# Optimization experiments

Hardware: AMD Instinct MI355X
Metric: run time of the kernel (lower is better)

## Reference

```python
import jax, jax.numpy as jnp
import numpy as np

B, S, D, H = 2, 2048, 1024, 16
HD = D // H  # per-head dim = 64


def setup_inputs() -> dict:
    key = jax.random.key(0)
    ks = jax.random.split(key, 9)
    s = 0.02
    return {
        "h": jax.random.normal(ks[0], (B, S, D), jnp.float32),
        "Wq": jax.random.normal(ks[1], (D, D), jnp.float32) * s,
        "bq": jax.random.normal(ks[2], (D,), jnp.float32) * s,
        "Wk": jax.random.normal(ks[3], (D, D), jnp.float32) * s,
        "bk": jax.random.normal(ks[4], (D,), jnp.float32) * s,
        "Wv": jax.random.normal(ks[5], (D, D), jnp.float32) * s,
        "bv": jax.random.normal(ks[6], (D,), jnp.float32) * s,
        "Wo": jax.random.normal(ks[7], (D, D), jnp.float32) * s,
        "bo": jax.random.normal(ks[8], (D,), jnp.float32) * s,
    }


def reference(h, Wq, bq, Wk, bk, Wv, bv, Wo, bo):
    b, s, d = h.shape
    # Linear projections (torch Linear: x @ W.T + b), split heads -> [B,H,S,HD]
    def split_heads(x):
        return x.reshape(b, s, H, HD).transpose(0, 2, 1, 3)

    q = split_heads(h @ Wq.T + bq)
    k = split_heads(h @ Wk.T + bk)
    v = split_heads(h @ Wv.T + bv)

    # scaled scores [B,H,S,S]
    qk = jnp.einsum("bhqd,bhkd->bhqk", q, k) / np.sqrt(HD).astype(np.float32)
    # causal mask: strictly upper triangle -> -inf
    causal = jnp.triu(jnp.ones((s, s), dtype=bool), k=1)
    qk = jnp.where(causal[None, None], -jnp.inf, qk)

    probs = jax.nn.softmax(qk, axis=-1)
    o = jnp.einsum("bhqk,bhkd->bhqd", probs, v)
    o = o.transpose(0, 2, 1, 3).reshape(b, s, d)
    return o @ Wo.T + bo
```

## Files before the change

### kernel.cpp

```cpp
#include <hip/hip_runtime.h>
#include <stdint.h>

typedef __bf16 bf16;
typedef __bf16 bf16x4_t __attribute__((ext_vector_type(4)));
typedef __bf16 bf16x8_t __attribute__((ext_vector_type(8)));
typedef float f32x4 __attribute__((ext_vector_type(4)));

static constexpr int NB = 2, SS = 2048, DD = 1024, NH = 16, HD = 64;

__device__ __forceinline__ void gl_lds16(const void* g, void* l) {
    __builtin_amdgcn_global_load_lds((__attribute__((address_space(1))) void*)g,
                                     (__attribute__((address_space(3))) void*)l, 16, 0, 0);
}

__global__ __launch_bounds__(256) void cast_all(const float* __restrict__ h,
                                                const float* __restrict__ Wq,
                                                const float* __restrict__ Wk,
                                                const float* __restrict__ Wv,
                                                const float* __restrict__ Wo,
                                                bf16* __restrict__ dst) {
    int i = blockIdx.x * 256 + threadIdx.x;
    const float* src;
    int off;
    if (i < 1048576) { src = h; off = i; }
    else {
        int r = i - 1048576;
        int w = r >> 18;
        off = r & 262143;
        src = (w == 0) ? Wq : (w == 1) ? Wk : (w == 2) ? Wv : Wo;
    }
    float4 v = reinterpret_cast<const float4*>(src)[off];
    bf16x4_t o;
    o.x = (bf16)v.x; o.y = (bf16)v.y; o.z = (bf16)v.z; o.w = (bf16)v.w;
    reinterpret_cast<bf16x4_t*>(dst)[i] = o;
}

__device__ __forceinline__ void gemm128_mainloop(const bf16* __restrict__ Ablk,
                                                 const bf16* __restrict__ Bblk,
                                                 int K, f32x4 acc[4][4]) {
    __shared__ __align__(16) bf16 As[128 * 32];
    __shared__ __align__(16) bf16 Bs[128 * 32];
    const int tid = threadIdx.x;
    const int wave = tid >> 6, lane = tid & 63;
    const int quad = lane >> 4, l15 = lane & 15;
    const int wm = wave >> 1, wn = wave & 1;

#pragma unroll
    for (int mi = 0; mi < 4; mi++)
#pragma unroll
        for (int ni = 0; ni < 4; ni++) {
            acc[mi][ni][0] = 0.f; acc[mi][ni][1] = 0.f;
            acc[mi][ni][2] = 0.f; acc[mi][ni][3] = 0.f;
        }

    const int n0c = tid;
    const int r0 = n0c >> 2, c0 = (n0c & 3) ^ ((r0 >> 1) & 3);
    const int n1c = 256 + tid;
    const int r1 = n1c >> 2, c1 = (n1c & 3) ^ ((r1 >> 1) & 3);

    for (int kk = 0; kk < K; kk += 32) {
        __syncthreads();
        gl_lds16(Ablk + (size_t)r0 * K + kk + c0 * 8, &As[(wave * 64) * 8]);
        gl_lds16(Ablk + (size_t)r1 * K + kk + c1 * 8, &As[(256 + wave * 64) * 8]);
        gl_lds16(Bblk + (size_t)r0 * K + kk + c0 * 8, &Bs[(wave * 64) * 8]);
        gl_lds16(Bblk + (size_t)r1 * K + kk + c1 * 8, &Bs[(256 + wave * 64) * 8]);
        __syncthreads();

        bf16x8_t a[4], b[4];
#pragma unroll
        for (int mi = 0; mi < 4; mi++) {
            int R = wm * 64 + mi * 16 + l15;
            a[mi] = *(const bf16x8_t*)&As[R * 32 + ((quad ^ ((R >> 1) & 3)) << 3)];
        }
#pragma unroll
        for (int ni = 0; ni < 4; ni++) {
            int R = wn * 64 + ni * 16 + l15;
            b[ni] = *(const bf16x8_t*)&Bs[R * 32 + ((quad ^ ((R >> 1) & 3)) << 3)];
        }
#pragma unroll
        for (int mi = 0; mi < 4; mi++)
#pragma unroll
            for (int ni = 0; ni < 4; ni++)
                acc[mi][ni] = __builtin_amdgcn_mfma_f32_16x16x32_bf16(a[mi], b[ni], acc[mi][ni], 0, 0, 0);
    }
}

__device__ __forceinline__ void gemm64_mainloop(const bf16* __restrict__ Ablk,
                                                const bf16* __restrict__ Bblk,
                                                int K, f32x4 acc[2][4]) {
    __shared__ __align__(16) bf16 As[64 * 32];
    __shared__ __align__(16) bf16 Bs[128 * 32];
    const int tid = threadIdx.x;
    const int wave = tid >> 6, lane = tid & 63;
    const int quad = lane >> 4, l15 = lane & 15;
    const int wm = wave >> 1, wn = wave & 1;

#pragma unroll
    for (int mi = 0; mi < 2; mi++)
#pragma unroll
        for (int ni = 0; ni < 4; ni++) {
            acc[mi][ni][0] = 0.f; acc[mi][ni][1] = 0.f;
            acc[mi][ni][2] = 0.f; acc[mi][ni][3] = 0.f;
        }

    const int ra = tid >> 2, ca = (tid & 3) ^ ((ra >> 1) & 3);
    const int r0 = tid >> 2, c0 = (tid & 3) ^ ((r0 >> 1) & 3);
    const int n1c = 256 + tid;
    const int r1 = n1c >> 2, c1 = (n1c & 3) ^ ((r1 >> 1) & 3);

    for (int kk = 0; kk < K; kk += 32) {
        __syncthreads();
        gl_lds16(Ablk + (size_t)ra * K + kk + ca * 8, &As[(wave * 64) * 8]);
        gl_lds16(Bblk + (size_t)r0 * K + kk + c0 * 8, &Bs[(wave * 64) * 8]);
        gl_lds16(Bblk + (size_t)r1 * K + kk + c1 * 8, &Bs[(256 + wave * 64) * 8]);
        __syncthreads();

        bf16x8_t a[2], b[4];
#pragma unroll
        for (int mi = 0; mi < 2; mi++) {
            int R = wm * 32 + mi * 16 + l15;
            a[mi] = *(const bf16x8_t*)&As[R * 32 + ((quad ^ ((R >> 1) & 3)) << 3)];
        }
#pragma unroll
        for (int ni = 0; ni < 4; ni++) {
            int R = wn * 64 + ni * 16 + l15;
            b[ni] = *(const bf16x8_t*)&Bs[R * 32 + ((quad ^ ((R >> 1) & 3)) << 3)];
        }
#pragma unroll
        for (int mi = 0; mi < 2; mi++)
#pragma unroll
            for (int ni = 0; ni < 4; ni++)
                acc[mi][ni] = __builtin_amdgcn_mfma_f32_16x16x32_bf16(a[mi], b[ni], acc[mi][ni], 0, 0, 0);
    }
}

__global__ __launch_bounds__(256) void gemm_qkv(const bf16* __restrict__ A, const bf16* __restrict__ Wqkv,
                                                const float* __restrict__ bq, const float* __restrict__ bk,
                                                const float* __restrict__ bv,
                                                bf16* __restrict__ Qb, bf16* __restrict__ Kb, bf16* __restrict__ Vb) {
    const int m0 = blockIdx.x * 128;
    const int n0 = blockIdx.y * 128;
    f32x4 acc[4][4];
    gemm128_mainloop(A + (size_t)m0 * DD, Wqkv + (size_t)n0 * DD, DD, acc);

    const int tid = threadIdx.x, wave = tid >> 6, lane = tid & 63;
    const int quad = lane >> 4, l15 = lane & 15;
    const int wm = wave >> 1, wn = wave & 1;

    const int which = n0 >> 10;
    const float* bias = (which == 0) ? bq : (which == 1) ? bk : bv;
    const float sc = (which == 0) ? 0.18033688f : 1.0f;

    const int cbase = (n0 & 1023) + wn * 64;
    const int head = cbase >> 6;
    const int bb = m0 >> 11;
    const int s0 = (m0 & 2047) + wm * 64;

    if (which == 2) {
        bf16* dbase = Vb + ((size_t)(bb * NH + head)) * HD * SS;
#pragma unroll
        for (int ni = 0; ni < 4; ni++) {
            float bsv = bias[cbase + ni * 16 + l15];
            int hd = ni * 16 + l15;
#pragma unroll
            for (int mi = 0; mi < 4; mi++) {
                bf16x4_t pb;
                pb.x = (bf16)(acc[mi][ni][0] + bsv);
                pb.y = (bf16)(acc[mi][ni][1] + bsv);
                pb.z = (bf16)(acc[mi][ni][2] + bsv);
                pb.w = (bf16)(acc[mi][ni][3] + bsv);
                int s = s0 + mi * 16 + quad * 4;
                *(bf16x4_t*)&dbase[(size_t)hd * SS + s] = pb;
            }
        }
    } else {
        bf16* dst = (which == 0) ? Qb : Kb;
        bf16* dbase = dst + ((size_t)(bb * NH + head)) * SS * HD;
#pragma unroll
        for (int ni = 0; ni < 4; ni++) {
            float bsv = bias[cbase + ni * 16 + l15];
            int hd = ni * 16 + l15;
#pragma unroll
            for (int mi = 0; mi < 4; mi++) {
#pragma unroll
                for (int r = 0; r < 4; r++) {
                    int s = s0 + mi * 16 + quad * 4 + r;
                    dbase[(size_t)s * HD + hd] = (bf16)((acc[mi][ni][r] + bsv) * sc);
                }
            }
        }
    }
}

__global__ __launch_bounds__(256) void gemm_out(const bf16* __restrict__ A, const bf16* __restrict__ Wo,
                                                const float* __restrict__ bo, float* __restrict__ out) {
    const int m0 = blockIdx.x * 64, n0 = blockIdx.y * 128;
    f32x4 acc[2][4];
    gemm64_mainloop(A + (size_t)m0 * DD, Wo + (size_t)n0 * DD, DD, acc);

    const int tid = threadIdx.x, wave = tid >> 6, lane = tid & 63;
    const int quad = lane >> 4, l15 = lane & 15;
    const int wm = wave >> 1, wn = wave & 1;
    float* obase = out + (size_t)(m0 + wm * 32) * DD + n0 + wn * 64;
#pragma unroll
    for (int ni = 0; ni < 4; ni++) {
        float bias = bo[n0 + wn * 64 + ni * 16 + l15];
#pragma unroll
        for (int mi = 0; mi < 2; mi++)
#pragma unroll
            for (int r = 0; r < 4; r++)
                obase[(size_t)(mi * 16 + quad * 4 + r) * DD + ni * 16 + l15] = acc[mi][ni][r] + bias;
    }
}

__global__ __launch_bounds__(256, 3) void attn_kernel(const bf16* __restrict__ Qb, const bf16* __restrict__ Kb,
                                                      const bf16* __restrict__ Vb, bf16* __restrict__ Ob,
                                                      bf16* __restrict__ Opart, float* __restrict__ Ml) {
    constexpr int PQ[24]  = {15,14,13,12,11,10, 9, 8, 15, 7, 14, 6, 13, 5, 12, 4, 11, 3, 10, 2,  9, 1,  8, 0};
    constexpr int PJ0[24] = { 0, 0, 0, 0, 0, 0, 0, 0,  8, 0,  8, 0,  8, 0,  8, 0,  8, 0,  8, 0,  8, 0,  8, 0};
    constexpr int PJ1[24] = { 8, 8, 8, 8, 8, 8, 8, 8, 16, 8, 15, 7, 14, 6, 13, 5, 12, 4, 11, 3, 10, 2,  9, 1};

    __shared__ __align__(16) bf16 Kt[128 * 64];
    __shared__ __align__(16) bf16 Vt[64 * 128];
    __shared__ __align__(16) bf16 Pt[4 * 32 * 64];

    const int tid = threadIdx.x, wave = tid >> 6, lane = tid & 63;
    const int quad = lane >> 4, l15 = lane & 15;
    const int bx = blockIdx.x;
    const int p = bx >> 5, bh = bx & 31;
    const int qtile = PQ[p], jbeg = PJ0[p], jend = PJ1[p];
    const bool diagpart = (jend == qtile + 1);
    const size_t hoff = (size_t)bh * SS * HD;
    const bf16* Qg = Qb + hoff + (size_t)qtile * 128 * HD;
    const bf16* Vbase = Vb + (size_t)bh * HD * SS;
    bf16* Pw = &Pt[wave * 2048];

    bf16x8_t qf[2][2];
#pragma unroll
    for (int qt = 0; qt < 2; qt++)
#pragma unroll
        for (int ks = 0; ks < 2; ks++)
            qf[qt][ks] = *(const bf16x8_t*)(Qg + (wave * 32 + qt * 16 + l15) * HD + ks * 32 + quad * 8);

    f32x4 o[2][4];
#pragma unroll
    for (int qt = 0; qt < 2; qt++)
#pragma unroll
        for (int nO = 0; nO < 4; nO++) {
            o[qt][nO][0] = 0.f; o[qt][nO][1] = 0.f; o[qt][nO][2] = 0.f; o[qt][nO][3] = 0.f;
        }
    float mrow[2] = {-__builtin_inff(), -__builtin_inff()};
    float lrow[2] = {0.f, 0.f};

    for (int j = jbeg; j < jend; j++) {
        __syncthreads();
        const bf16* Kg = Kb + hoff + (size_t)j * 128 * HD;
#pragma unroll
        for (int t = 0; t < 4; t++) {
            int n = t * 256 + tid;
            int row = n >> 3, gc = (n & 7) ^ (row & 7);
            gl_lds16(Kg + row * HD + gc * 8, &Kt[(t * 256 + wave * 64) * 8]);
        }
        const bf16* Vg = Vbase + j * 128;
#pragma unroll
        for (int t = 0; t < 4; t++) {
            int n = t * 256 + tid;
            int row = n >> 4, gc = (n & 15) ^ (row & 15);
            gl_lds16(Vg + (size_t)row * SS + gc * 8, &Vt[(t * 256 + wave * 64) * 8]);
        }
        __syncthreads();

        const bool diag = diagpart && (j == jend - 1);
#pragma unroll 1
        for (int kh = 0; kh < 2; kh++) {
            if (diag && kh == 1 && wave < 2) break;

            f32x4 st[4][2];
#pragma unroll
            for (int kt = 0; kt < 4; kt++)
#pragma unroll
                for (int qt = 0; qt < 2; qt++) {
                    st[kt][qt][0] = 0.f; st[kt][qt][1] = 0.f; st[kt][qt][2] = 0.f; st[kt][qt][3] = 0.f;
                }
#pragma unroll
            for (int ks = 0; ks < 2; ks++) {
#pragma unroll
                for (int kt = 0; kt < 4; kt++) {
                    int R = (kh * 4 + kt) * 16 + l15;
                    bf16x8_t kf = *(const bf16x8_t*)&Kt[R * HD + ((((ks << 2) | quad) ^ (R & 7)) << 3)];
#pragma unroll
                    for (int qt = 0; qt < 2; qt++)
                        st[kt][qt] = __builtin_amdgcn_mfma_f32_16x16x32_bf16(kf, qf[qt][ks], st[kt][qt], 0, 0, 0);
                }
            }
            if (diag) {
#pragma unroll
                for (int kt = 0; kt < 4; kt++)
#pragma unroll
                    for (int qt = 0; qt < 2; qt++)
#pragma unroll
                        for (int r = 0; r < 4; r++) {
                            int key = kh * 64 + kt * 16 + quad * 4 + r;
                            int row = wave * 32 + qt * 16 + l15;
                            if (key > row) st[kt][qt][r] = -__builtin_inff();
                        }
            }

#pragma unroll
            for (int qt = 0; qt < 2; qt++) {
                float mx = -__builtin_inff();
#pragma unroll
                for (int kt = 0; kt < 4; kt++)
#pragma unroll
                    for (int r = 0; r < 4; r++) mx = fmaxf(mx, st[kt][qt][r]);
                mx = fmaxf(mx, __shfl_xor(mx, 16));
                mx = fmaxf(mx, __shfl_xor(mx, 32));
                float mnew = fmaxf(mrow[qt], mx);
                float alpha = exp2f(mrow[qt] - mnew);
                mrow[qt] = mnew;
                float sum = 0.f;
                const int row = qt * 16 + l15;
#pragma unroll
                for (int kt = 0; kt < 4; kt++) {
                    float p0 = exp2f(st[kt][qt][0] - mnew);
                    float p1 = exp2f(st[kt][qt][1] - mnew);
                    float p2 = exp2f(st[kt][qt][2] - mnew);
                    float p3 = exp2f(st[kt][qt][3] - mnew);
                    sum += (p0 + p1) + (p2 + p3);
                    bf16x4_t pb;
                    pb.x = (bf16)p0; pb.y = (bf16)p1; pb.z = (bf16)p2; pb.w = (bf16)p3;
                    int c = kt * 2 + (quad >> 1);
                    *(bf16x4_t*)&Pw[row * 64 + ((c ^ (row & 7)) << 3) + ((quad & 1) << 2)] = pb;
                }
                sum += __shfl_xor(sum, 16);
                sum += __shfl_xor(sum, 32);
                lrow[qt] = lrow[qt] * alpha + sum;
#pragma unroll
                for (int r = 0; r < 4; r++) {
                    float a = __shfl(alpha, (lane & 48) | (quad * 4 + r));
#pragma unroll
                    for (int nO = 0; nO < 4; nO++) o[qt][nO][r] *= a;
                }
            }

#pragma unroll
            for (int ks = 0; ks < 2; ks++) {
                bf16x8_t pf[2];
#pragma unroll
                for (int qt = 0; qt < 2; qt++) {
                    int row = qt * 16 + l15;
                    int c = (ks << 2) | quad;
                    pf[qt] = *(const bf16x8_t*)&Pw[row * 64 + ((c ^ (row & 7)) << 3)];
                }
#pragma unroll
                for (int nO = 0; nO < 4; nO++) {
                    int c = kh * 8 + ks * 4 + quad;
                    bf16x8_t vf = *(const bf16x8_t*)&Vt[(nO * 16 + l15) * 128 + ((c ^ l15) << 3)];
#pragma unroll
                    for (int qt = 0; qt < 2; qt++)
                        o[qt][nO] = __builtin_amdgcn_mfma_f32_16x16x32_bf16(pf[qt], vf, o[qt][nO], 0, 0, 0);
                }
            }
        }
    }

    const int bb = bh >> 4, hh = bh & 15;
    if (qtile >= 8) {
        const int pidx = ((bh << 3) + (qtile - 8)) * 2 + (jbeg != 0 ? 1 : 0);
        bf16* Op = Opart + (size_t)pidx * (128 * 64);
        float* mlp = Ml + (size_t)pidx * 256;
#pragma unroll
        for (int qt = 0; qt < 2; qt++) {
            if (quad == 0) {
                mlp[wave * 32 + qt * 16 + l15] = mrow[qt];
                mlp[128 + wave * 32 + qt * 16 + l15] = lrow[qt];
            }
#pragma unroll
            for (int r = 0; r < 4; r++) {
                int row = wave * 32 + qt * 16 + quad * 4 + r;
#pragma unroll
                for (int nO = 0; nO < 4; nO++)
                    Op[row * 64 + nO * 16 + l15] = (bf16)o[qt][nO][r];
            }
        }
    } else {
#pragma unroll
        for (int qt = 0; qt < 2; qt++) {
#pragma unroll
            for (int r = 0; r < 4; r++) {
                float linv = 1.f / __shfl(lrow[qt], (lane & 48) | (quad * 4 + r));
                int srow = qtile * 128 + wave * 32 + qt * 16 + quad * 4 + r;
#pragma unroll
                for (int nO = 0; nO < 4; nO++)
                    Ob[((size_t)(bb * SS + srow)) * DD + hh * HD + nO * 16 + l15] = (bf16)(o[qt][nO][r] * linv);
            }
        }
    }
}

__global__ __launch_bounds__(256) void merge_kernel(const bf16* __restrict__ Opart,
                                                    const float* __restrict__ Ml,
                                                    bf16* __restrict__ Ob) {
    const int bh = blockIdx.x >> 3, q8 = blockIdx.x & 7;
    const int p0 = ((bh << 3) + q8) * 2, p1 = p0 + 1;
    const int t = threadIdx.x, row = t >> 1, c0 = (t & 1) * 32;
    float m0 = Ml[p0 * 256 + row], l0 = Ml[p0 * 256 + 128 + row];
    float m1 = Ml[p1 * 256 + row], l1 = Ml[p1 * 256 + 128 + row];
    float M = fmaxf(m0, m1);
    float w0 = exp2f(m0 - M), w1 = exp2f(m1 - M);
    float inv = 1.f / (l0 * w0 + l1 * w1);
    w0 *= inv; w1 *= inv;
    const bf16* O0 = Opart + (size_t)p0 * (128 * 64) + row * 64 + c0;
    const bf16* O1 = Opart + (size_t)p1 * (128 * 64) + row * 64 + c0;
    const int bb = bh >> 4, hh = bh & 15;
    const int srow = (8 + q8) * 128 + row;
    bf16* dst = Ob + ((size_t)(bb * SS + srow)) * DD + hh * HD + c0;
#pragma unroll
    for (int i = 0; i < 4; i++) {
        bf16x8_t a = *(const bf16x8_t*)(O0 + i * 8);
        bf16x8_t b = *(const bf16x8_t*)(O1 + i * 8);
        bf16x8_t r;
#pragma unroll
        for (int jj = 0; jj < 8; jj++)
            r[jj] = (bf16)((float)a[jj] * w0 + (float)b[jj] * w1);
        *(bf16x8_t*)(dst + i * 8) = r;
    }
}

extern "C" void kernel_launch(void* const* d_in, const int* in_sizes, int n_in,
                              void* d_out, int out_size, void* d_ws, size_t ws_size,
                              hipStream_t stream) {
    (void)in_sizes; (void)n_in; (void)out_size; (void)ws_size;
    const float* h  = (const float*)d_in[0];
    const float* Wq = (const float*)d_in[1];
    const float* bq = (const float*)d_in[2];
    const float* Wk = (const float*)d_in[3];
    const float* bk = (const float*)d_in[4];
    const float* Wv = (const float*)d_in[5];
    const float* bv = (const float*)d_in[6];
    const float* Wo = (const float*)d_in[7];
    const float* bo = (const float*)d_in[8];
    float* out = (float*)d_out;

    char* ws = (char*)d_ws;
    bf16* hbf  = (bf16*)(ws);
    bf16* wqkv = (bf16*)(ws + 8388608);
    bf16* wo   = (bf16*)(ws + 8388608 + 6291456);
    bf16* Qb   = (bf16*)(ws + 16777216);
    bf16* Kb   = (bf16*)(ws + 16777216 + 8388608);
    bf16* Vb   = (bf16*)(ws + 16777216 + 2 * 8388608);
    bf16* Ob   = (bf16*)(ws + 16777216 + 3 * 8388608);
    bf16*  Opart = (bf16*)(ws);
    float* Ml    = (float*)(ws + 8388608);

    cast_all<<<8192, 256, 0, stream>>>(h, Wq, Wk, Wv, Wo, hbf);
    gemm_qkv<<<dim3(32, 24), 256, 0, stream>>>(hbf, wqkv, bq, bk, bv, Qb, Kb, Vb);
    attn_kernel<<<768, 256, 0, stream>>>(Qb, Kb, Vb, Ob, Opart, Ml);
    merge_kernel<<<256, 256, 0, stream>>>(Opart, Ml, Ob);
    gemm_out<<<dim3(64, 8), 256, 0, stream>>>(Ob, wo, bo, out);
}
```

Measured before the change: 187.9 us.

## Deepen GEMM K-tile to 64 and transpose PV MFMA for vectorized epilogue

```diff
diff --git a/kernel.cpp b/kernel.cpp
--- a/kernel.cpp
+++ b/kernel.cpp
@@ -38,8 +38,8 @@
 __device__ __forceinline__ void gemm128_mainloop(const bf16* __restrict__ Ablk,
                                                  const bf16* __restrict__ Bblk,
                                                  int K, f32x4 acc[4][4]) {
-    __shared__ __align__(16) bf16 As[128 * 32];
-    __shared__ __align__(16) bf16 Bs[128 * 32];
+    __shared__ __align__(16) bf16 As[128 * 64];
+    __shared__ __align__(16) bf16 Bs[128 * 64];
     const int tid = threadIdx.x;
     const int wave = tid >> 6, lane = tid & 63;
     const int quad = lane >> 4, l15 = lane & 15;
@@ -53,43 +53,50 @@
             acc[mi][ni][2] = 0.f; acc[mi][ni][3] = 0.f;
         }
 
-    const int n0c = tid;
-    const int r0 = n0c >> 2, c0 = (n0c & 3) ^ ((r0 >> 1) & 3);
-    const int n1c = 256 + tid;
-    const int r1 = n1c >> 2, c1 = (n1c & 3) ^ ((r1 >> 1) & 3);
-
-    for (int kk = 0; kk < K; kk += 32) {
+    int rr[4], cc[4];
+#pragma unroll
+    for (int n = 0; n < 4; n++) {
+        int cid = n * 256 + tid;
+        rr[n] = cid >> 3;
+        cc[n] = (cid & 7) ^ (rr[n] & 7);
+    }
+
+    for (int kk = 0; kk < K; kk += 64) {
         __syncthreads();
-        gl_lds16(Ablk + (size_t)r0 * K + kk + c0 * 8, &As[(wave * 64) * 8]);
-        gl_lds16(Ablk + (size_t)r1 * K + kk + c1 * 8, &As[(256 + wave * 64) * 8]);
-        gl_lds16(Bblk + (size_t)r0 * K + kk + c0 * 8, &Bs[(wave * 64) * 8]);
-        gl_lds16(Bblk + (size_t)r1 * K + kk + c1 * 8, &Bs[(256 + wave * 64) * 8]);
+#pragma unroll
+        for (int n = 0; n < 4; n++) {
+            gl_lds16(Ablk + (size_t)rr[n] * K + kk + cc[n] * 8, &As[(n * 256 + wave * 64) * 8]);
+            gl_lds16(Bblk + (size_t)rr[n] * K + kk + cc[n] * 8, &Bs[(n * 256 + wave * 64) * 8]);
+        }
         __syncthreads();
 
-        bf16x8_t a[4], b[4];
-#pragma unroll
-        for (int mi = 0; mi < 4; mi++) {
-            int R = wm * 64 + mi * 16 + l15;
-            a[mi] = *(const bf16x8_t*)&As[R * 32 + ((quad ^ ((R >> 1) & 3)) << 3)];
-        }
-#pragma unroll
-        for (int ni = 0; ni < 4; ni++) {
-            int R = wn * 64 + ni * 16 + l15;
-            b[ni] = *(const bf16x8_t*)&Bs[R * 32 + ((quad ^ ((R >> 1) & 3)) << 3)];
-        }
-#pragma unroll
-        for (int mi = 0; mi < 4; mi++)
-#pragma unroll
-            for (int ni = 0; ni < 4; ni++)
-                acc[mi][ni] = __builtin_amdgcn_mfma_f32_16x16x32_bf16(a[mi], b[ni], acc[mi][ni], 0, 0, 0);
+#pragma unroll
+        for (int ks = 0; ks < 2; ks++) {
+            bf16x8_t a[4], b[4];
+#pragma unroll
+            for (int mi = 0; mi < 4; mi++) {
+                int R = wm * 64 + mi * 16 + l15;
+                a[mi] = *(const bf16x8_t*)&As[R * 64 + ((((ks << 2) | quad) ^ (R & 7)) << 3)];
+            }
+#pragma unroll
+            for (int ni = 0; ni < 4; ni++) {
+                int R = wn * 64 + ni * 16 + l15;
+                b[ni] = *(const bf16x8_t*)&Bs[R * 64 + ((((ks << 2) | quad) ^ (R & 7)) << 3)];
+            }
+#pragma unroll
+            for (int mi = 0; mi < 4; mi++)
+#pragma unroll
+                for (int ni = 0; ni < 4; ni++)
+                    acc[mi][ni] = __builtin_amdgcn_mfma_f32_16x16x32_bf16(a[mi], b[ni], acc[mi][ni], 0, 0, 0);
+        }
     }
 }
 
 __device__ __forceinline__ void gemm64_mainloop(const bf16* __restrict__ Ablk,
                                                 const bf16* __restrict__ Bblk,
                                                 int K, f32x4 acc[2][4]) {
-    __shared__ __align__(16) bf16 As[64 * 32];
-    __shared__ __align__(16) bf16 Bs[128 * 32];
+    __shared__ __align__(16) bf16 As[64 * 64];
+    __shared__ __align__(16) bf16 Bs[128 * 64];
     const int tid = threadIdx.x;
     const int wave = tid >> 6, lane = tid & 63;
     const int quad = lane >> 4, l15 = lane & 15;
@@ -103,34 +110,49 @@
             acc[mi][ni][2] = 0.f; acc[mi][ni][3] = 0.f;
         }
 
-    const int ra = tid >> 2, ca = (tid & 3) ^ ((ra >> 1) & 3);
-    const int r0 = tid >> 2, c0 = (tid & 3) ^ ((r0 >> 1) & 3);
-    const int n1c = 256 + tid;
-    const int r1 = n1c >> 2, c1 = (n1c & 3) ^ ((r1 >> 1) & 3);
-
-    for (int kk = 0; kk < K; kk += 32) {
+    int ra[2], ca[2], rb[4], cb[4];
+#pragma unroll
+    for (int n = 0; n < 2; n++) {
+        int cid = n * 256 + tid;
+        ra[n] = cid >> 3;
+        ca[n] = (cid & 7) ^ (ra[n] & 7);
+    }
+#pragma unroll
+    for (int n = 0; n < 4; n++) {
+        int cid = n * 256 + tid;
+        rb[n] = cid >> 3;
+        cb[n] = (cid & 7) ^ (rb[n] & 7);
+    }
+
+    for (int kk = 0; kk < K; kk += 64) {
         __syncthreads();
-        gl_lds16(Ablk + (size_t)ra * K + kk + ca * 8, &As[(wave * 64) * 8]);
-        gl_lds16(Bblk + (size_t)r0 * K + kk + c0 * 8, &Bs[(wave * 64) * 8]);
-        gl_lds16(Bblk + (size_t)r1 * K + kk + c1 * 8, &Bs[(256 + wave * 64) * 8]);
+#pragma unroll
+        for (int n = 0; n < 2; n++)
+            gl_lds16(Ablk + (size_t)ra[n] * K + kk + ca[n] * 8, &As[(n * 256 + wave * 64) * 8]);
+#pragma unroll
+        for (int n = 0; n < 4; n++)
+            gl_lds16(Bblk + (size_t)rb[n] * K + kk + cb[n] * 8, &Bs[(n * 256 + wave * 64) * 8]);
         __syncthreads();
 
-        bf16x8_t a[2], b[4];
-#pragma unroll
-        for (int mi = 0; mi < 2; mi++) {
-            int R = wm * 32 + mi * 16 + l15;
-            a[mi] = *(const bf16x8_t*)&As[R * 32 + ((quad ^ ((R >> 1) & 3)) << 3)];
-        }
-#pragma unroll
-        for (int ni = 0; ni < 4; ni++) {
-            int R = wn * 64 + ni * 16 + l15;
-            b[ni] = *(const bf16x8_t*)&Bs[R * 32 + ((quad ^ ((R >> 1) & 3)) << 3)];
-        }
-#pragma unroll
-        for (int mi = 0; mi < 2; mi++)
-#pragma unroll
-            for (int ni = 0; ni < 4; ni++)
-                acc[mi][ni] = __builtin_amdgcn_mfma_f32_16x16x32_bf16(a[mi], b[ni], acc[mi][ni], 0, 0, 0);
+#pragma unroll
+        for (int ks = 0; ks < 2; ks++) {
+            bf16x8_t a[2], b[4];
+#pragma unroll
+            for (int mi = 0; mi < 2; mi++) {
+                int R = wm * 32 + mi * 16 + l15;
+                a[mi] = *(const bf16x8_t*)&As[R * 64 + ((((ks << 2) | quad) ^ (R & 7)) << 3)];
+            }
+#pragma unroll
+            for (int ni = 0; ni < 4; ni++) {
+                int R = wn * 64 + ni * 16 + l15;
+                b[ni] = *(const bf16x8_t*)&Bs[R * 64 + ((((ks << 2) | quad) ^ (R & 7)) << 3)];
+            }
+#pragma unroll
+            for (int mi = 0; mi < 2; mi++)
+#pragma unroll
+                for (int ni = 0; ni < 4; ni++)
+                    acc[mi][ni] = __builtin_amdgcn_mfma_f32_16x16x32_bf16(a[mi], b[ni], acc[mi][ni], 0, 0, 0);
+        }
     }
 }
 
@@ -246,8 +268,8 @@
 #pragma unroll
     for (int qt = 0; qt < 2; qt++)
 #pragma unroll
-        for (int nO = 0; nO < 4; nO++) {
-            o[qt][nO][0] = 0.f; o[qt][nO][1] = 0.f; o[qt][nO][2] = 0.f; o[qt][nO][3] = 0.f;
+        for (int dt = 0; dt < 4; dt++) {
+            o[qt][dt][0] = 0.f; o[qt][dt][1] = 0.f; o[qt][dt][2] = 0.f; o[qt][dt][3] = 0.f;
         }
     float mrow[2] = {-__builtin_inff(), -__builtin_inff()};
     float lrow[2] = {0.f, 0.f};
@@ -336,11 +358,7 @@
                 sum += __shfl_xor(sum, 32);
                 lrow[qt] = lrow[qt] * alpha + sum;
 #pragma unroll
-                for (int r = 0; r < 4; r++) {
-                    float a = __shfl(alpha, (lane & 48) | (quad * 4 + r));
-#pragma unroll
-                    for (int nO = 0; nO < 4; nO++) o[qt][nO][r] *= a;
-                }
+                for (int dt = 0; dt < 4; dt++) o[qt][dt] *= alpha;
             }
 
 #pragma unroll
@@ -353,46 +371,69 @@
                     pf[qt] = *(const bf16x8_t*)&Pw[row * 64 + ((c ^ (row & 7)) << 3)];
                 }
 #pragma unroll
-                for (int nO = 0; nO < 4; nO++) {
+                for (int dt = 0; dt < 4; dt++) {
                     int c = kh * 8 + ks * 4 + quad;
-                    bf16x8_t vf = *(const bf16x8_t*)&Vt[(nO * 16 + l15) * 128 + ((c ^ l15) << 3)];
+                    bf16x8_t vf = *(const bf16x8_t*)&Vt[(dt * 16 + l15) * 128 + ((c ^ l15) << 3)];
 #pragma unroll
                     for (int qt = 0; qt < 2; qt++)
-                        o[qt][nO] = __builtin_amdgcn_mfma_f32_16x16x32_bf16(pf[qt], vf, o[qt][nO], 0, 0, 0);
+                        o[qt][dt] = __builtin_amdgcn_mfma_f32_16x16x32_bf16(vf, pf[qt], o[qt][dt], 0, 0, 0);
                 }
             }
         }
     }
 
     const int bb = bh >> 4, hh = bh & 15;
-    if (qtile >= 8) {
+    const bool split = (qtile >= 8);
+    float scl[2];
+#pragma unroll
+    for (int qt = 0; qt < 2; qt++) scl[qt] = split ? 1.f : (1.f / lrow[qt]);
+
+    if (split) {
         const int pidx = ((bh << 3) + (qtile - 8)) * 2 + (jbeg != 0 ? 1 : 0);
-        bf16* Op = Opart + (size_t)pidx * (128 * 64);
         float* mlp = Ml + (size_t)pidx * 256;
-#pragma unroll
-        for (int qt = 0; qt < 2; qt++) {
-            if (quad == 0) {
+        if (quad == 0) {
+#pragma unroll
+            for (int qt = 0; qt < 2; qt++) {
                 mlp[wave * 32 + qt * 16 + l15] = mrow[qt];
                 mlp[128 + wave * 32 + qt * 16 + l15] = lrow[qt];
             }
-#pragma unroll
-            for (int r = 0; r < 4; r++) {
-                int row = wave * 32 + qt * 16 + quad * 4 + r;
-#pragma unroll
-                for (int nO = 0; nO < 4; nO++)
-                    Op[row * 64 + nO * 16 + l15] = (bf16)o[qt][nO][r];
-            }
-        }
-    } else {
-#pragma unroll
-        for (int qt = 0; qt < 2; qt++) {
-#pragma unroll
-            for (int r = 0; r < 4; r++) {
-                float linv = 1.f / __shfl(lrow[qt], (lane & 48) | (quad * 4 + r));
-                int srow = qtile * 128 + wave * 32 + qt * 16 + quad * 4 + r;
-#pragma unroll
-                for (int nO = 0; nO < 4; nO++)
-                    Ob[((size_t)(bb * SS + srow)) * DD + hh * HD + nO * 16 + l15] = (bf16)(o[qt][nO][r] * linv);
+        }
+    }
+#pragma unroll
+    for (int qt = 0; qt < 2; qt++) {
+        const int row = qt * 16 + l15;
+#pragma unroll
+        for (int dt = 0; dt < 4; dt++) {
+            bf16x4_t pb;
+            pb.x = (bf16)(o[qt][dt][0] * scl[qt]);
+            pb.y = (bf16)(o[qt][dt][1] * scl[qt]);
+            pb.z = (bf16)(o[qt][dt][2] * scl[qt]);
+            pb.w = (bf16)(o[qt][dt][3] * scl[qt]);
+            int c = dt * 2 + (quad >> 1);
+            *(bf16x4_t*)&Pw[row * 64 + ((c ^ (row & 7)) << 3) + ((quad & 1) << 2)] = pb;
+        }
+    }
+    {
+        const int rl = lane >> 1;
+        const int half = lane & 1;
+        const int q = wave * 32 + rl;
+        if (split) {
+            const int pidx = ((bh << 3) + (qtile - 8)) * 2 + (jbeg != 0 ? 1 : 0);
+            bf16* Op = Opart + (size_t)pidx * (128 * 64);
+#pragma unroll
+            for (int i = 0; i < 4; i++) {
+                int dc = half * 4 + i;
+                bf16x8_t v = *(const bf16x8_t*)&Pw[rl * 64 + ((dc ^ (rl & 7)) << 3)];
+                *(bf16x8_t*)&Op[q * 64 + dc * 8] = v;
+            }
+        } else {
+            const int srow = qtile * 128 + q;
+            bf16* dst = Ob + ((size_t)(bb * SS + srow)) * DD + hh * HD;
+#pragma unroll
+            for (int i = 0; i < 4; i++) {
+                int dc = half * 4 + i;
+                bf16x8_t v = *(const bf16x8_t*)&Pw[rl * 64 + ((dc ^ (rl & 7)) << 3)];
+                *(bf16x8_t*)&dst[dc * 8] = v;
             }
         }
     }
```

New measurement: 198.2 us. 5.5% more time.

## Fuse split-KV merge into output projection GEMM and swizzle QKV block order

Applied to the files above, without the earlier changes.

```diff
diff --git a/kernel.cpp b/kernel.cpp
--- a/kernel.cpp
+++ b/kernel.cpp
@@ -85,61 +85,16 @@
     }
 }
 
-__device__ __forceinline__ void gemm64_mainloop(const bf16* __restrict__ Ablk,
-                                                const bf16* __restrict__ Bblk,
-                                                int K, f32x4 acc[2][4]) {
-    __shared__ __align__(16) bf16 As[64 * 32];
-    __shared__ __align__(16) bf16 Bs[128 * 32];
-    const int tid = threadIdx.x;
-    const int wave = tid >> 6, lane = tid & 63;
-    const int quad = lane >> 4, l15 = lane & 15;
-    const int wm = wave >> 1, wn = wave & 1;
-
-#pragma unroll
-    for (int mi = 0; mi < 2; mi++)
-#pragma unroll
-        for (int ni = 0; ni < 4; ni++) {
-            acc[mi][ni][0] = 0.f; acc[mi][ni][1] = 0.f;
-            acc[mi][ni][2] = 0.f; acc[mi][ni][3] = 0.f;
-        }
-
-    const int ra = tid >> 2, ca = (tid & 3) ^ ((ra >> 1) & 3);
-    const int r0 = tid >> 2, c0 = (tid & 3) ^ ((r0 >> 1) & 3);
-    const int n1c = 256 + tid;
-    const int r1 = n1c >> 2, c1 = (n1c & 3) ^ ((r1 >> 1) & 3);
-
-    for (int kk = 0; kk < K; kk += 32) {
-        __syncthreads();
-        gl_lds16(Ablk + (size_t)ra * K + kk + ca * 8, &As[(wave * 64) * 8]);
-        gl_lds16(Bblk + (size_t)r0 * K + kk + c0 * 8, &Bs[(wave * 64) * 8]);
-        gl_lds16(Bblk + (size_t)r1 * K + kk + c1 * 8, &Bs[(256 + wave * 64) * 8]);
-        __syncthreads();
-
-        bf16x8_t a[2], b[4];
-#pragma unroll
-        for (int mi = 0; mi < 2; mi++) {
-            int R = wm * 32 + mi * 16 + l15;
-            a[mi] = *(const bf16x8_t*)&As[R * 32 + ((quad ^ ((R >> 1) & 3)) << 3)];
-        }
-#pragma unroll
-        for (int ni = 0; ni < 4; ni++) {
-            int R = wn * 64 + ni * 16 + l15;
-            b[ni] = *(const bf16x8_t*)&Bs[R * 32 + ((quad ^ ((R >> 1) & 3)) << 3)];
-        }
-#pragma unroll
-        for (int mi = 0; mi < 2; mi++)
-#pragma unroll
-            for (int ni = 0; ni < 4; ni++)
-                acc[mi][ni] = __builtin_amdgcn_mfma_f32_16x16x32_bf16(a[mi], b[ni], acc[mi][ni], 0, 0, 0);
-    }
-}
-
 __global__ __launch_bounds__(256) void gemm_qkv(const bf16* __restrict__ A, const bf16* __restrict__ Wqkv,
                                                 const float* __restrict__ bq, const float* __restrict__ bk,
                                                 const float* __restrict__ bv,
                                                 bf16* __restrict__ Qb, bf16* __restrict__ Kb, bf16* __restrict__ Vb) {
-    const int m0 = blockIdx.x * 128;
-    const int n0 = blockIdx.y * 128;
+    const int g = blockIdx.x + 32 * blockIdx.y;
+    const int c = g & 7, i = g >> 3;
+    const int xm = (c & 3) * 8 + (i & 7);
+    const int yn = (c >> 2) * 12 + (i >> 3);
+    const int m0 = xm * 128;
+    const int n0 = yn * 128;
     f32x4 acc[4][4];
     gemm128_mainloop(A + (size_t)m0 * DD, Wqkv + (size_t)n0 * DD, DD, acc);
 
@@ -192,15 +147,92 @@
     }
 }
 
-__global__ __launch_bounds__(256) void gemm_out(const bf16* __restrict__ A, const bf16* __restrict__ Wo,
+__global__ __launch_bounds__(256) void gemm_out(const bf16* __restrict__ Ob, const bf16* __restrict__ Opart,
+                                                const float* __restrict__ Ml, const bf16* __restrict__ Wo,
                                                 const float* __restrict__ bo, float* __restrict__ out) {
+    __shared__ __align__(16) bf16 As[64 * 32];
+    __shared__ __align__(16) bf16 Bs[128 * 32];
     const int m0 = blockIdx.x * 64, n0 = blockIdx.y * 128;
-    f32x4 acc[2][4];
-    gemm64_mainloop(A + (size_t)m0 * DD, Wo + (size_t)n0 * DD, DD, acc);
-
-    const int tid = threadIdx.x, wave = tid >> 6, lane = tid & 63;
+    const int tid = threadIdx.x;
+    const int wave = tid >> 6, lane = tid & 63;
     const int quad = lane >> 4, l15 = lane & 15;
     const int wm = wave >> 1, wn = wave & 1;
+
+    f32x4 acc[2][4];
+#pragma unroll
+    for (int mi = 0; mi < 2; mi++)
+#pragma unroll
+        for (int ni = 0; ni < 4; ni++) {
+            acc[mi][ni][0] = 0.f; acc[mi][ni][1] = 0.f;
+            acc[mi][ni][2] = 0.f; acc[mi][ni][3] = 0.f;
+        }
+
+    const int ra = tid >> 2, ca = (tid & 3) ^ ((ra >> 1) & 3);
+    const int r0 = tid >> 2, c0 = (tid & 3) ^ ((r0 >> 1) & 3);
+    const int n1c = 256 + tid;
+    const int r1 = n1c >> 2, c1 = (n1c & 3) ^ ((r1 >> 1) & 3);
+
+    const int lr = m0 & 2047;
+    const bool split = (lr >= 1024);
+    const int bb = m0 >> 11;
+    const int q8 = (lr - 1024) >> 7;
+    const int prow = ((lr - 1024) & 127) + ra;
+    const bf16* Ablk = Ob + (size_t)m0 * DD;
+    const bf16* Bblk = Wo + (size_t)n0 * DD;
+
+    float w0 = 0.f, w1 = 0.f;
+    int hh_cur = -1;
+
+    for (int kk = 0; kk < DD; kk += 32) {
+        __syncthreads();
+        if (!split) {
+            gl_lds16(Ablk + (size_t)ra * DD + kk + ca * 8, &As[(wave * 64) * 8]);
+        } else {
+            const int hh = kk >> 6;
+            const int pidx = (((bb * 16 + hh) << 3) + q8) * 2;
+            if (hh != hh_cur) {
+                hh_cur = hh;
+                float m0v = Ml[pidx * 256 + prow];
+                float l0v = Ml[pidx * 256 + 128 + prow];
+                float m1v = Ml[(pidx + 1) * 256 + prow];
+                float l1v = Ml[(pidx + 1) * 256 + 128 + prow];
+                float M = fmaxf(m0v, m1v);
+                float e0 = exp2f(m0v - M), e1 = exp2f(m1v - M);
+                float inv = 1.f / (l0v * e0 + l1v * e1);
+                w0 = e0 * inv; w1 = e1 * inv;
+            }
+            const int col64 = (kk & 32) + ca * 8;
+            const bf16* O0 = Opart + (size_t)pidx * 8192 + (prow << 6) + col64;
+            bf16x8_t a0 = *(const bf16x8_t*)O0;
+            bf16x8_t a1 = *(const bf16x8_t*)(O0 + 8192);
+            bf16x8_t mg;
+#pragma unroll
+            for (int jj = 0; jj < 8; jj++)
+                mg[jj] = (bf16)((float)a0[jj] * w0 + (float)a1[jj] * w1);
+            *(bf16x8_t*)&As[tid * 8] = mg;
+        }
+        gl_lds16(Bblk + (size_t)r0 * DD + kk + c0 * 8, &Bs[(wave * 64) * 8]);
+        gl_lds16(Bblk + (size_t)r1 * DD + kk + c1 * 8, &Bs[(256 + wave * 64) * 8]);
+        __syncthreads();
+
+        bf16x8_t a[2], b[4];
+#pragma unroll
+        for (int mi = 0; mi < 2; mi++) {
+            int R = wm * 32 + mi * 16 + l15;
+            a[mi] = *(const bf16x8_t*)&As[R * 32 + ((quad ^ ((R >> 1) & 3)) << 3)];
+        }
+#pragma unroll
+        for (int ni = 0; ni < 4; ni++) {
+            int R = wn * 64 + ni * 16 + l15;
+            b[ni] = *(const bf16x8_t*)&Bs[R * 32 + ((quad ^ ((R >> 1) & 3)) << 3)];
+        }
+#pragma unroll
+        for (int mi = 0; mi < 2; mi++)
+#pragma unroll
+            for (int ni = 0; ni < 4; ni++)
+                acc[mi][ni] = __builtin_amdgcn_mfma_f32_16x16x32_bf16(a[mi], b[ni], acc[mi][ni], 0, 0, 0);
+    }
+
     float* obase = out + (size_t)(m0 + wm * 32) * DD + n0 + wn * 64;
 #pragma unroll
     for (int ni = 0; ni < 4; ni++) {
@@ -395,35 +427,6 @@
                     Ob[((size_t)(bb * SS + srow)) * DD + hh * HD + nO * 16 + l15] = (bf16)(o[qt][nO][r] * linv);
             }
         }
-    }
-}
-
-__global__ __launch_bounds__(256) void merge_kernel(const bf16* __restrict__ Opart,
-                                                    const float* __restrict__ Ml,
-                                                    bf16* __restrict__ Ob) {
-    const int bh = blockIdx.x >> 3, q8 = blockIdx.x & 7;
-    const int p0 = ((bh << 3) + q8) * 2, p1 = p0 + 1;
-    const int t = threadIdx.x, row = t >> 1, c0 = (t & 1) * 32;
-    float m0 = Ml[p0 * 256 + row], l0 = Ml[p0 * 256 + 128 + row];
-    float m1 = Ml[p1 * 256 + row], l1 = Ml[p1 * 256 + 128 + row];
-    float M = fmaxf(m0, m1);
-    float w0 = exp2f(m0 - M), w1 = exp2f(m1 - M);
-    float inv = 1.f / (l0 * w0 + l1 * w1);
-    w0 *= inv; w1 *= inv;
-    const bf16* O0 = Opart + (size_t)p0 * (128 * 64) + row * 64 + c0;
-    const bf16* O1 = Opart + (size_t)p1 * (128 * 64) + row * 64 + c0;
-    const int bb = bh >> 4, hh = bh & 15;
-    const int srow = (8 + q8) * 128 + row;
-    bf16* dst = Ob + ((size_t)(bb * SS + srow)) * DD + hh * HD + c0;
-#pragma unroll
-    for (int i = 0; i < 4; i++) {
-        bf16x8_t a = *(const bf16x8_t*)(O0 + i * 8);
-        bf16x8_t b = *(const bf16x8_t*)(O1 + i * 8);
-        bf16x8_t r;
-#pragma unroll
-        for (int jj = 0; jj < 8; jj++)
-            r[jj] = (bf16)((float)a[jj] * w0 + (float)b[jj] * w1);
-        *(bf16x8_t*)(dst + i * 8) = r;
     }
 }
 
@@ -456,6 +459,5 @@
     cast_all<<<8192, 256, 0, stream>>>(h, Wq, Wk, Wv, Wo, hbf);
     gemm_qkv<<<dim3(32, 24), 256, 0, stream>>>(hbf, wqkv, bq, bk, bv, Qb, Kb, Vb);
     attn_kernel<<<768, 256, 0, stream>>>(Qb, Kb, Vb, Ob, Opart, Ml);
-    merge_kernel<<<256, 256, 0, stream>>>(Opart, Ml, Ob);
-    gemm_out<<<dim3(64, 8), 256, 0, stream>>>(Ob, wo, bo, out);
-}
+    gemm_out<<<dim3(64, 8), 256, 0, stream>>>(Ob, Opart, Ml, wo, bo, out);
+}
```

Result: slower. 196.3 us (+4.4%).
